# Kernel tuning notes

Hardware: AMD Instinct MI355X
Metric: run time of the kernel (lower is better)

Reference implementation:

```python
import jax, jax.numpy as jnp
import numpy as np

B, S, F, I, E, TOP_K, K, D, CLASSES = 2, 2048, 512, 1024, 8, 2, 7, 2, 8192
BETA = 0.9
INIT_SCALE = D ** -0.5


def setup_inputs() -> dict:
    key = jax.random.key(0)
    ks = jax.random.split(key, 10)
    s = lambda *shape: shape
    return {
        "inp": jax.random.randint(ks[0], (B, S), 0, CLASSES),
        "embed": jax.random.normal(ks[1], (CLASSES, 2 * F), jnp.float32) * 0.02,
        "gate_in_w": jax.random.normal(ks[2], (D, F, E), jnp.float32) * (F ** -0.5),
        "w_in": jax.random.normal(ks[3], (D, E, F, I), jnp.float32) * (F ** -0.5),
        "conv_w": jax.random.normal(ks[4], (D, I, I, K), jnp.float32) * ((I * K) ** -0.5),
        "gate_out_w": jax.random.normal(ks[5], (D, I, E), jnp.float32) * (I ** -0.5),
        "w_out": jax.random.normal(ks[6], (D, E, I, 3 * F), jnp.float32) * (I ** -0.5),
        "out_w": jax.random.normal(ks[7], (CLASSES, 2 * F), jnp.float32) * ((2 * F) ** -0.5),
        "out_b": jnp.zeros((CLASSES,), jnp.float32),
    }


def _moe(x, gate_w, expert_w):
    # x: [T, Fin]; NaiveGate top-k routing + grouped-GEMM combine.
    logits = x @ gate_w                                  # [T, E]
    top_vals, top_idx = jax.lax.top_k(logits, TOP_K)     # [T, k]
    scores = jax.nn.softmax(top_vals, axis=-1)           # softmax over selected experts
    n_exp = gate_w.shape[1]
    combine = jnp.sum(scores[:, :, None] * jax.nn.one_hot(top_idx, n_exp, dtype=x.dtype), axis=1)  # [T, E]
    y = jnp.einsum("tf,efo->teo", x, expert_w)           # dense all-expert eval
    return jnp.einsum("teo,te->to", y, combine)


def _norm(out):
    # custom norm over channel dim (dim 1 of [B, C, S])
    out = out - out.mean(axis=1, keepdims=True)
    c = out.shape[1]
    return out / (jnp.linalg.norm(out, axis=1, keepdims=True) * (c ** -0.5) + 1e-5)


def _cell(x, gate_in, win, cw, gate_out, wout, divisor):
    # x: [B, F, S]
    b, f, seq = x.shape
    t = x.transpose(0, 2, 1).reshape(b * seq, f)
    h = jax.nn.relu(_moe(t, gate_in, win))               # [T, I]
    h = h.reshape(b, seq, -1).transpose(0, 2, 1)         # [B, I, S]
    # causal depthwise-style conv (groups=1), left-pad K-1
    h = jax.lax.conv_general_dilated(h, cw, (1,), [(cw.shape[-1] - 1, 0)],
                                     dimension_numbers=("NCH", "OIH", "NCH"))
    h = jax.nn.relu(h)
    t2 = h.transpose(0, 2, 1).reshape(b * seq, -1)
    o = _moe(t2, gate_out, wout).reshape(b, seq, 3 * f).transpose(0, 2, 1)  # [B, 3F, S]
    depth_, scale, shift = jnp.split(o, 3, axis=1)
    cum = jnp.cumsum(depth_, axis=2)                      # running sum over sequence
    out = cum / divisor * scale + shift
    return _norm(out) * INIT_SCALE


def reference(inp, embed, gate_in_w, w_in, conv_w, gate_out_w, w_out, out_w, out_b):
    emb = embed[inp]                                      # [B, S, 2F]
    x = emb.transpose(0, 2, 1)                            # [B, 2F, S]
    x0, x1 = x[:, :F], x[:, F:]
    divisor = (jnp.arange(S, dtype=x.dtype) + 1.0)[None, None, :]
    for d in range(D):
        # momentum coupling with LinearAttentionCell
        f = _cell(x1, gate_in_w[d], w_in[d], conv_w[d], gate_out_w[d], w_out[d], divisor)
        y = x0 * BETA + f * (1.0 - BETA)
        x0, x1 = x1, y
        # additive coupling with Identity
        y = x0 + x1
        x0, x1 = x1, y
    out = jnp.concatenate([x0, x1], axis=1)               # [B, 2F, S]
    logits = jnp.einsum("bcs,kc->bks", out, out_w) + out_b[None, :, None]
    return logits
```

## Files before the change

### kernel.cpp

```cpp
#include <hip/hip_runtime.h>
#include <math.h>

typedef unsigned short u16;
typedef unsigned int   u32;

#define B_ 2
#define S_ 2048
#define F_ 512
#define I_ 1024
#define E_ 8
#define KW_ 7
#define D_ 2
#define CLASSES_ 8192
#define T_ (B_*S_)
#define SP_ (S_+6)
#define NSLOT_ 9216
#define GMAX_ 72

typedef __bf16 bf16x8 __attribute__((ext_vector_type(8)));
typedef float  f32x4  __attribute__((ext_vector_type(4)));

__device__ __forceinline__ u16 f2b(float f) {
    u32 x = __float_as_uint(f);
    return (u16)((x + 0x7fffu + ((x >> 16) & 1u)) >> 16);
}
__device__ __forceinline__ void fsplit(float v, u16& h, u16& l) {
    u16 hh = f2b(v);
    float hv = __uint_as_float(((u32)hh) << 16);
    h = hh;
    l = f2b(v - hv);
}

template<int N> __device__ __forceinline__ void waitvm() {
    asm volatile("s_waitcnt vmcnt(%0)" :: "n"(N) : "memory");
}

#define GLDS16(g, l) __builtin_amdgcn_global_load_lds( \
    (const __attribute__((address_space(1))) u32*)(g), \
    (__attribute__((address_space(3))) u32*)(l), 16, 0, 0)

__global__ void embed_k(const int* __restrict__ inp, const float* __restrict__ emb,
                        float* __restrict__ X0, float* __restrict__ X1)
{
    int t = blockIdx.x;
    int r = inp[t];
    const float* e = emb + (size_t)r * (2*F_);
    for (int c = threadIdx.x; c < F_; c += 256) {
        X0[(size_t)t*F_ + c] = e[c];
        X1[(size_t)t*F_ + c] = e[F_ + c];
    }
}

__global__ void initslot_k(int* __restrict__ stok, int* __restrict__ cnt)
{
    int i = blockIdx.x*256 + threadIdx.x;
    if (i < NSLOT_) stok[i] = -1;
    if (i < E_) cnt[i] = 0;
}

template<int MODE, int W>
__global__ __launch_bounds__(512) void gatev_k(const float* __restrict__ X,
                                               const float* __restrict__ X2,
                                               const float* __restrict__ GW,
                                               int2* __restrict__ e2, float2* __restrict__ w2,
                                               int* __restrict__ cnt)
{
    __shared__ float gw[W*E_];
    for (int i = threadIdx.x; i < W*E_; i += 512) {
        int f = i >> 3, e = i & 7;
        gw[e*W + f] = GW[i];
    }
    __syncthreads();
    int wv = threadIdx.x >> 6, l = threadIdx.x & 63;
    int t = blockIdx.x * 8 + wv;
    const float* xr  = X + (size_t)t * W;
    const float* x2r = MODE ? (X2 + (size_t)t * W) : nullptr;
    float a[8];
    #pragma unroll
    for (int e = 0; e < 8; e++) a[e] = 0.f;
    #pragma unroll
    for (int c = 0; c < W/256; c++) {
        int f = c*256 + l*4;
        float4 x = *(const float4*)(xr + f);
        if (MODE) {
            float4 y = *(const float4*)(x2r + f);
            x.x = fmaxf(x.x + y.x, 0.f); x.y = fmaxf(x.y + y.y, 0.f);
            x.z = fmaxf(x.z + y.z, 0.f); x.w = fmaxf(x.w + y.w, 0.f);
        }
        #pragma unroll
        for (int e = 0; e < 8; e++) {
            float4 g = *(const float4*)(gw + e*W + f);
            a[e] += x.x*g.x + x.y*g.y + x.z*g.z + x.w*g.w;
        }
    }
    #pragma unroll
    for (int e = 0; e < 8; e++) {
        #pragma unroll
        for (int off = 32; off; off >>= 1) a[e] += __shfl_xor(a[e], off);
    }
    if (l == 0) {
        float v0 = -3.4e38f, v1 = -3.4e38f; int i0 = 0, i1 = 0;
        #pragma unroll
        for (int k = 0; k < E_; k++) {
            float v = a[k];
            if (v > v0)      { v1 = v0; i1 = i0; v0 = v; i0 = k; }
            else if (v > v1) { v1 = v;  i1 = k; }
        }
        float ex = expf(v1 - v0);
        e2[t] = make_int2(i0, i1);
        w2[t] = make_float2(1.f/(1.f+ex), ex/(1.f+ex));
        atomicAdd(&cnt[i0], 1);
        atomicAdd(&cnt[i1], 1);
    }
}

__global__ __launch_bounds__(256) void schedscat_k(const int* __restrict__ cnt,
                                                   const int2* __restrict__ e2,
                                                   const float2* __restrict__ w2,
                                                   int4* __restrict__ s0, int4* __restrict__ s1,
                                                   int split,
                                                   int* __restrict__ stok, float* __restrict__ sw)
{
    __shared__ int lpos[E_];
    int tid = threadIdx.x;
    int nb[E_], slotst[E_], gst[E_];
    int poff = 0, g0 = 0, g1 = 0;
    #pragma unroll
    for (int e = 0; e < E_; e++) {
        int n = (cnt[e] + 127) >> 7;
        nb[e] = n;
        slotst[e] = poff;
        if (e < split) { gst[e] = g0; g0 += n; }
        else           { gst[e] = g1; g1 += n; }
        poff += n << 7;
    }
    if (tid < E_) lpos[tid] = slotst[tid];
    if (tid < GMAX_) {
        int4 en = make_int4(0,0,0,0);
        for (int e = 0; e < split; e++)
            if (tid >= gst[e] && tid < gst[e] + nb[e])
                en = make_int4(slotst[e] + (tid - gst[e])*128, e, 1, 0);
        s0[tid] = en;
    }
    if (split < E_ && tid >= 128 && tid < 128 + GMAX_) {
        int j = tid - 128;
        int4 en = make_int4(0,0,0,0);
        for (int e = split; e < E_; e++)
            if (j >= gst[e] && j < gst[e] + nb[e])
                en = make_int4(slotst[e] + (j - gst[e])*128, e - split, 1, 0);
        s1[j] = en;
    }
    __syncthreads();
    for (int t = tid; t < T_; t += 256) {
        int2 e = e2[t]; float2 w = w2[t];
        int p0 = atomicAdd(&lpos[e.x], 1);
        stok[p0] = t;          sw[p0] = w.x;
        int p1 = atomicAdd(&lpos[e.y], 1);
        stok[p1] = t | 4096;   sw[p1] = w.y;
    }
}

__global__ __launch_bounds__(256) void transp_k(const float* __restrict__ src0,
                                                u16* __restrict__ dh, u16* __restrict__ dl,
                                                int R, int C)
{
    __shared__ float tl[32][33];
    int z = blockIdx.z;
    const float* src = src0 + (size_t)z * R * C;
    size_t dbase = (size_t)z * R * C;
    int c0 = blockIdx.x * 32, r0 = blockIdx.y * 32;
    int tx = threadIdx.x & 31, ty = threadIdx.x >> 5;
    #pragma unroll
    for (int j = 0; j < 32; j += 8)
        tl[ty + j][tx] = src[(size_t)(r0 + ty + j) * C + c0 + tx];
    __syncthreads();
    #pragma unroll
    for (int j = 0; j < 32; j += 8) {
        u16 h, l; fsplit(tl[tx][ty + j], h, l);
        size_t idx = dbase + (size_t)(c0 + ty + j) * R + r0 + tx;
        dh[idx] = h; dl[idx] = l;
    }
}

__global__ __launch_bounds__(256) void convw_k(const float* __restrict__ src,
                                               u16* __restrict__ dh, u16* __restrict__ dl)
{
    __shared__ float row[KW_*I_];
    int o = blockIdx.x;
    const float* s = src + (size_t)o * (KW_*I_);
    for (int c = threadIdx.x; c < KW_*I_; c += 256) row[c] = s[c];
    __syncthreads();
    size_t base = (size_t)o * (KW_*I_);
    for (int j = threadIdx.x; j < KW_*I_; j += 256) {
        int kc = j >> 10, i = j & 1023;
        u16 h, l; fsplit(row[i*KW_ + kc], h, l);
        dh[base + j] = h; dl[base + j] = l;
    }
}

__global__ void split_k(const float* __restrict__ src, u16* __restrict__ dh, u16* __restrict__ dl)
{
    size_t i = ((size_t)blockIdx.x * 256 + threadIdx.x) * 4;
    float4 v = *(const float4*)(src + i);
    ushort4 oh, ol;
    fsplit(v.x, oh.x, ol.x); fsplit(v.y, oh.y, ol.y);
    fsplit(v.z, oh.z, ol.z); fsplit(v.w, oh.w, ol.w);
    *(ushort4*)(dh + i) = oh;
    *(ushort4*)(dl + i) = ol;
}

__global__ void hsplit_k(const float* __restrict__ Ha, const float* __restrict__ Hb,
                         u16* __restrict__ ph, u16* __restrict__ pl)
{
    int gid = blockIdx.x*256 + threadIdx.x;
    int eb = gid * 4;
    int t = eb >> 10, c = eb & 1023;
    float4 a = *(const float4*)(Ha + eb);
    float4 b = *(const float4*)(Hb + eb);
    ushort4 hh, ll;
    fsplit(fmaxf(a.x+b.x,0.f), hh.x, ll.x); fsplit(fmaxf(a.y+b.y,0.f), hh.y, ll.y);
    fsplit(fmaxf(a.z+b.z,0.f), hh.z, ll.z); fsplit(fmaxf(a.w+b.w,0.f), hh.w, ll.w);
    size_t row = (size_t)(t >> 11)*SP_ + 6 + (t & (S_-1));
    *(ushort4*)(ph + (row << 10) + c) = hh;
    *(ushort4*)(pl + (row << 10) + c) = ll;
}

__global__ void crelu_k(const float* __restrict__ a0, const float* __restrict__ a1,
                        u16* __restrict__ dh, u16* __restrict__ dl)
{
    size_t i = ((size_t)blockIdx.x * 256 + threadIdx.x) * 4;
    float4 a = *(const float4*)(a0 + i);
    float4 b = *(const float4*)(a1 + i);
    ushort4 hh, ll;
    fsplit(fmaxf(a.x+b.x,0.f), hh.x, ll.x); fsplit(fmaxf(a.y+b.y,0.f), hh.y, ll.y);
    fsplit(fmaxf(a.z+b.z,0.f), hh.z, ll.z); fsplit(fmaxf(a.w+b.w,0.f), hh.w, ll.w);
    *(ushort4*)(dh + i) = hh;
    *(ushort4*)(dl + i) = ll;
}

__global__ void hpadzero_k(u16* __restrict__ ph, u16* __restrict__ pl)
{
    int idx = blockIdx.x*256 + threadIdx.x;
    int b = idx / (6*I_);
    int rem = idx - b*(6*I_);
    size_t a = ((size_t)b*SP_ + (rem >> 10))*I_ + (rem & 1023);
    ph[a] = 0; pl[a] = 0;
}

enum { A_SPLIT=0, A_CONV=1, A_GATHER2=2 };
enum { EP_RANK=0, EP_DUAL=1, EP_FINAL=2 };

#define SBSZ(Pv) ((((Pv)==3)?16384:8192) + 8192*(((Pv)>=2)?2:1))

template<int AM, int EP, int PASSES>
__global__ __launch_bounds__(256, ((2*SBSZ(PASSES)) <= 32768) ? 4 : (((2*SBSZ(PASSES)) <= 49152) ? 3 : 2))
void mgemm(const void* __restrict__ A1, const void* __restrict__ A2,
           const u16* __restrict__ Bh, const u16* __restrict__ Bl,
           float* __restrict__ Ca, float* __restrict__ Cb,
           int N, int Kd, int ldb,
           const int4* __restrict__ sched, const int* __restrict__ stok,
           const float* __restrict__ sw, const float* __restrict__ bias)
{
    constexpr bool HAL = (PASSES==3);
    constexpr bool HBL = (PASSES>=2);
    constexpr int OAL  = 8192;
    constexpr int OBH  = (HAL ? 16384 : 8192);
    constexpr int OBL  = OBH + 8192;
    constexpr int SB   = OBH + 8192*(HBL ? 2 : 1);
    constexpr int NLOADS = 2*(HBL ? 2 : 1) + 2*(HAL ? 2 : 1);
    __shared__ uint4 ldsv[2*SB/16];
    char* lds = (char*)ldsv;

    const int tid  = threadIdx.x;
    const int lane = tid & 63, wid = tid >> 6;
    const int n0 = blockIdx.x * 128;

    int slot0 = 0, m0 = 0, koff = 0, kz = 0;
    const u16 *bhb = Bh, *blb = Bl;
    if (AM == A_GATHER2) {
        int4 sc = sched[blockIdx.y];
        if (!sc.z) return;
        slot0 = sc.x;
        size_t wo = (size_t)sc.y * N * ldb;
        bhb = Bh + wo; blb = Bl + wo;
    } else if (AM == A_CONV) {
        m0 = (blockIdx.y & 31) * 128;
        kz = blockIdx.y >> 5;
        koff = kz * Kd;
    } else {
        m0 = blockIdx.y * 128;
    }

    int srow[2], klog[2];
    #pragma unroll
    for (int c = 0; c < 2; c++) {
        int row = (tid >> 2) + c*64;
        srow[c] = row;
        klog[c] = ((tid & 3) ^ ((row >> 1) & 3)) << 3;
    }

    const u16 *bgh[2], *bgl[2];
    #pragma unroll
    for (int c = 0; c < 2; c++) {
        size_t off = (size_t)(n0 + srow[c]) * ldb + koff + klog[c];
        bgh[c] = bhb + off;
        bgl[c] = blb + off;
    }

    const u16 *a1p[2], *a2p[2];
    #pragma unroll
    for (int c = 0; c < 2; c++) {
        if (AM == A_SPLIT) {
            size_t off = (size_t)(m0 + srow[c]) * Kd + klog[c];
            a1p[c] = (const u16*)A1 + off;
            a2p[c] = (const u16*)A2 + off;
        } else if (AM == A_CONV) {
            int t = m0 + srow[c];
            size_t rb = (((size_t)(t >> 11)*SP_ + (t & (S_-1))) << 10) + koff + klog[c];
            a1p[c] = (const u16*)A1 + rb;
            a2p[c] = (const u16*)A2 + rb;
        } else {
            int s = stok[slot0 + srow[c]];
            int tk = (s < 0) ? 0 : (s & 4095);
            size_t off = (size_t)tk * Kd + klog[c];
            a1p[c] = (const u16*)A1 + off;
            a2p[c] = (const u16*)A2 + off;
        }
    }

    const int wr = wid >> 1, wc = wid & 1;
    const int l15 = lane & 15, kq = lane >> 4;
    int aoff[4], boff[4];
    #pragma unroll
    for (int m = 0; m < 4; m++) {
        int ra = wr*64 + m*16 + l15;
        aoff[m] = ra*64 + ((kq ^ ((ra >> 1) & 3)) << 4);
    }
    #pragma unroll
    for (int n = 0; n < 4; n++) {
        int rb = wc*64 + n*16 + l15;
        boff[n] = rb*64 + ((kq ^ ((rb >> 1) & 3)) << 4);
    }

    f32x4 acc[4][4];
    #pragma unroll
    for (int m = 0; m < 4; m++)
        #pragma unroll
        for (int n = 0; n < 4; n++) acc[m][n] = {0.f,0.f,0.f,0.f};

    const int nt = Kd >> 5;

#define STAGE_GL(K0, BB)                                                          \
    {                                                                             \
        _Pragma("unroll")                                                         \
        for (int c = 0; c < 2; c++) {                                             \
            GLDS16(bgh[c] + (K0), lds + (BB) + OBH + c*4096 + (wid<<10));         \
            if (HBL)                                                              \
                GLDS16(bgl[c] + (K0), lds + (BB) + OBL + c*4096 + (wid<<10));     \
        }                                                                         \
        _Pragma("unroll")                                                         \
        for (int c = 0; c < 2; c++) {                                             \
            GLDS16(a1p[c] + (K0), lds + (BB) + c*4096 + (wid<<10));               \
            if (HAL)                                                              \
                GLDS16(a2p[c] + (K0), lds + (BB) + OAL + c*4096 + (wid<<10));     \
        }                                                                         \
    }

    STAGE_GL(0, 0);
    STAGE_GL(32, SB);
    waitvm<NLOADS>();
    __builtin_amdgcn_s_barrier();

    for (int it = 0; it < nt; ++it) {
        const int bb = (it & 1) * SB;
        {
            bf16x8 ah[4], al[4], bhf[4], blf[4];
            #pragma unroll
            for (int m = 0; m < 4; m++) {
                ah[m] = *(const bf16x8*)(lds + bb + aoff[m]);
                if (HAL) al[m] = *(const bf16x8*)(lds + bb + OAL + aoff[m]);
            }
            #pragma unroll
            for (int n = 0; n < 4; n++) {
                bhf[n] = *(const bf16x8*)(lds + bb + OBH + boff[n]);
                if (HBL) blf[n] = *(const bf16x8*)(lds + bb + OBL + boff[n]);
            }
            #pragma unroll
            for (int m = 0; m < 4; m++)
                #pragma unroll
                for (int n = 0; n < 4; n++) {
                    acc[m][n] = __builtin_amdgcn_mfma_f32_16x16x32_bf16(ah[m], bhf[n], acc[m][n], 0, 0, 0);
                    if (HAL)
                        acc[m][n] = __builtin_amdgcn_mfma_f32_16x16x32_bf16(al[m], bhf[n], acc[m][n], 0, 0, 0);
                    if (HBL)
                        acc[m][n] = __builtin_amdgcn_mfma_f32_16x16x32_bf16(ah[m], blf[n], acc[m][n], 0, 0, 0);
                }
        }
        asm volatile("s_waitcnt lgkmcnt(0)" ::: "memory");
        __builtin_amdgcn_sched_barrier(0);
        __builtin_amdgcn_s_barrier();
        if (it + 2 < nt) {
            STAGE_GL((it + 2) << 5, bb);
            waitvm<NLOADS>();
            __builtin_amdgcn_s_barrier();
        } else if (it + 1 < nt) {
            waitvm<0>();
            __builtin_amdgcn_s_barrier();
        }
    }

    #pragma unroll
    for (int m = 0; m < 4; m++) {
        #pragma unroll
        for (int n = 0; n < 4; n++) {
            f32x4 v = acc[m][n];
            int rl0 = wr*64 + m*16 + (lane >> 4)*4;
            int col = n0 + wc*64 + n*16 + l15;
            #pragma unroll
            for (int j = 0; j < 4; j++) {
                float x = v[j];
                int rl = rl0 + j;
                if (EP == EP_RANK) {
                    int s = stok[slot0 + rl];
                    if (s >= 0) {
                        int tt = s & 4095;
                        float ww = sw[slot0 + rl];
                        float* dst = (s & 4096) ? Cb : Ca;
                        dst[(size_t)tt * N + col] = ww * x;
                    }
                } else if (EP == EP_DUAL) {
                    int r = m0 + rl;
                    float* dst = kz ? Cb : Ca;
                    dst[(size_t)r * N + col] = x;
                } else {
                    int r = m0 + rl;
                    x += bias[r];
                    int b = col >> 11, s = col & (S_-1);
                    Ca[(((size_t)(b*CLASSES_ + r)) << 11) + s] = x;
                }
            }
        }
    }
#undef STAGE_GL
}

#define SC_ 128
#define NCH_ (S_/SC_)
__global__ void cum1(const float* __restrict__ Oa, const float* __restrict__ Ob,
                     float* __restrict__ CS)
{
    int blk = blockIdx.x;
    int b = blk / NCH_, ch = blk % NCH_;
    int c = threadIdx.x;
    int s0 = ch * SC_;
    size_t base = ((size_t)(b*S_ + s0)) * (3*F_) + c;
    float sum = 0.f;
    for (int s = 0; s < SC_; s++) {
        size_t idx = base + (size_t)s * (3*F_);
        sum += Oa[idx] + Ob[idx];
    }
    CS[(size_t)blk * F_ + c] = sum;
}
__global__ void cum23(const float* __restrict__ Oa, const float* __restrict__ Ob,
                      const float* __restrict__ CS, float* __restrict__ FP)
{
    int blk = blockIdx.x;
    int b = blk / NCH_, ch = blk % NCH_;
    int c = threadIdx.x;
    float run = 0.f;
    for (int j = 0; j < ch; j++) run += CS[(size_t)(b*NCH_ + j) * F_ + c];
    int s0 = ch * SC_;
    for (int s = s0; s < s0 + SC_; s++) {
        size_t t = (size_t)b * S_ + s;
        size_t ro = t * (3*F_);
        run += Oa[ro + c] + Ob[ro + c];
        float scl = Oa[ro + F_ + c] + Ob[ro + F_ + c];
        float shf = Oa[ro + 2*F_ + c] + Ob[ro + 2*F_ + c];
        FP[t*F_ + c] = run / (float)(s + 1) * scl + shf;
    }
}

__global__ __launch_bounds__(256) void normupd_k(const float* __restrict__ FP,
                                                 float* __restrict__ X0, float* __restrict__ X1)
{
    __shared__ float sb[4];
    int t = blockIdx.x;
    const float* row = FP + (size_t)t * F_;
    int tid = threadIdx.x;
    float v0 = row[tid], v1 = row[tid + 256];
    float s = v0 + v1;
    #pragma unroll
    for (int off = 32; off; off >>= 1) s += __shfl_xor(s, off);
    int w = tid >> 6;
    if ((tid & 63) == 0) sb[w] = s;
    __syncthreads();
    float mean = (sb[0] + sb[1] + sb[2] + sb[3]) * (1.0f / F_);
    v0 -= mean; v1 -= mean;
    float q = v0*v0 + v1*v1;
    #pragma unroll
    for (int off = 32; off; off >>= 1) q += __shfl_xor(q, off);
    __syncthreads();
    if ((tid & 63) == 0) sb[w] = q;
    __syncthreads();
    float ss = sb[0] + sb[1] + sb[2] + sb[3];
    float denom = sqrtf(ss) * 0.04419417382415922f + 1e-5f;
    float sc = 0.70710678118654752f / denom;
    float f0 = v0 * sc, f1 = v1 * sc;
    size_t i0 = (size_t)t * F_ + tid, i1 = i0 + 256;
    float a0 = 0.9f * X0[i0] + 0.1f * f0;
    float a1 = 0.9f * X0[i1] + 0.1f * f1;
    X0[i0] = a0; X1[i0] += a0;
    X0[i1] = a1; X1[i1] += a1;
}

__global__ void concat_k(const float* __restrict__ X0, const float* __restrict__ X1,
                         u16* __restrict__ Xh, u16* __restrict__ Xl)
{
    int t = blockIdx.x;
    for (int c = threadIdx.x; c < F_; c += 256) {
        u16 h, l;
        fsplit(X0[(size_t)t*F_ + c], h, l);
        Xh[(size_t)t*(2*F_) + c] = h;      Xl[(size_t)t*(2*F_) + c] = l;
        fsplit(X1[(size_t)t*F_ + c], h, l);
        Xh[(size_t)t*(2*F_) + F_ + c] = h; Xl[(size_t)t*(2*F_) + F_ + c] = l;
    }
}

extern "C" void kernel_launch(void* const* d_in, const int* in_sizes, int n_in,
                              void* d_out, int out_size, void* d_ws, size_t ws_size,
                              hipStream_t stream)
{
    const int*   inp    = (const int*)  d_in[0];
    const float* embed  = (const float*)d_in[1];
    const float* gin_w  = (const float*)d_in[2];
    const float* w_in   = (const float*)d_in[3];
    const float* conv_w = (const float*)d_in[4];
    const float* gout_w = (const float*)d_in[5];
    const float* w_out  = (const float*)d_in[6];
    const float* out_w  = (const float*)d_in[7];
    const float* out_b  = (const float*)d_in[8];
    float* out = (float*)d_out;

    char* w = (char*)d_ws;
    auto alloc = [&](size_t bytes) { char* r = w; w += (bytes + 255) & ~(size_t)255; return r; };
    float* X0    = (float*)alloc((size_t)T_*F_*4);
    float* X1    = (float*)alloc((size_t)T_*F_*4);
    u16*   Hpadh = (u16*)  alloc((size_t)B_*SP_*I_*2);
    u16*   Hpadl = (u16*)  alloc((size_t)B_*SP_*I_*2);
    u16*   HCh   = (u16*)  alloc((size_t)T_*I_*2);
    u16*   HCl   = (u16*)  alloc((size_t)T_*I_*2);
    float* FP    = (float*)alloc((size_t)T_*F_*4);
    float* CS    = (float*)alloc((size_t)B_*NCH_*F_*4);
    char*  ar1   = alloc((size_t)T_*3*F_*4);
    char*  ar2   = alloc((size_t)T_*I_*4);
    char*  altr  = alloc((size_t)T_*3*F_*4);
    u16*   Wh    = (u16*)  alloc((size_t)I_*KW_*I_*2);
    u16*   Wl    = (u16*)  alloc((size_t)I_*KW_*I_*2);
    int2*  e2    = (int2*) alloc((size_t)T_*8);
    float2* w2   = (float2*)alloc((size_t)T_*8);
    int*   stok  = (int*)  alloc((size_t)NSLOT_*4);
    float* sw    = (float*)alloc((size_t)NSLOT_*4);
    int*   cnt   = (int*)  alloc(64);
    int4*  s0    = (int4*) alloc((size_t)GMAX_*16);
    int4*  s1    = (int4*) alloc((size_t)GMAX_*16);

    float* Ha  = (float*)ar1;
    float* Oa  = (float*)ar1;
    float* HC0 = (float*)ar2;
    float* Hb  = (float*)altr;
    float* HC1 = (float*)altr;
    float* Ob  = (float*)altr;
    u16*   X1h = (u16*)FP;
    u16*   X1l = X1h + (size_t)T_*F_;

    embed_k<<<T_, 256, 0, stream>>>(inp, embed, X0, X1);
    hpadzero_k<<<(B_*6*I_)/256, 256, 0, stream>>>(Hpadh, Hpadl);

    for (int d = 0; d < D_; ++d) {
        initslot_k<<<(NSLOT_+255)/256, 256, 0, stream>>>(stok, cnt);
        gatev_k<0, F_><<<T_/8, 512, 0, stream>>>(X1, nullptr, gin_w + (size_t)d*F_*E_, e2, w2, cnt);
        schedscat_k<<<1, 256, 0, stream>>>(cnt, e2, w2, s0, s1, 8, stok, sw);
        split_k<<<(T_*F_)/1024, 256, 0, stream>>>(X1, X1h, X1l);
        transp_k<<<dim3(I_/32, F_/32, E_), 256, 0, stream>>>(
            w_in + (size_t)d*E_*F_*I_, Wh, Wl, F_, I_);
        mgemm<A_GATHER2, EP_RANK, 3><<<dim3(I_/128, GMAX_), 256, 0, stream>>>(
            X1h, X1l, Wh, Wl, Ha, Hb, I_, F_, F_, s0, stok, sw, nullptr);
        hsplit_k<<<T_*I_/1024, 256, 0, stream>>>(Ha, Hb, Hpadh, Hpadl);

        convw_k<<<I_, 256, 0, stream>>>(conv_w + (size_t)d*I_*I_*KW_, Wh, Wl);
        mgemm<A_CONV, EP_DUAL, 3><<<dim3(I_/128, 64), 256, 0, stream>>>(
            Hpadh, Hpadl, Wh, Wl, HC0, HC1, I_, (KW_*I_)/2, KW_*I_, nullptr, nullptr, nullptr, nullptr);
        crelu_k<<<T_*I_/1024, 256, 0, stream>>>(HC0, HC1, HCh, HCl);

        initslot_k<<<(NSLOT_+255)/256, 256, 0, stream>>>(stok, cnt);
        gatev_k<1, I_><<<T_/8, 512, 0, stream>>>(HC0, HC1, gout_w + (size_t)d*I_*E_, e2, w2, cnt);
        schedscat_k<<<1, 256, 0, stream>>>(cnt, e2, w2, s0, s1, 4, stok, sw);
        for (int c = 0; c < 2; ++c) {
            transp_k<<<dim3((3*F_)/32, I_/32, 4), 256, 0, stream>>>(
                w_out + (size_t)d*E_*I_*(3*F_) + (size_t)c*4*I_*(3*F_), Wh, Wl, I_, 3*F_);
            const int4* sc = (c == 0) ? s0 : s1;
            if (d == 0)
                mgemm<A_GATHER2, EP_RANK, 3><<<dim3((3*F_)/128, GMAX_), 256, 0, stream>>>(
                    HCh, HCl, Wh, Wl, Oa, Ob, 3*F_, I_, I_, sc, stok, sw, nullptr);
            else
                mgemm<A_GATHER2, EP_RANK, 1><<<dim3((3*F_)/128, GMAX_), 256, 0, stream>>>(
                    HCh, HCl, Wh, Wl, Oa, Ob, 3*F_, I_, I_, sc, stok, sw, nullptr);
        }

        cum1<<<B_*NCH_, F_, 0, stream>>>(Oa, Ob, CS);
        cum23<<<B_*NCH_, F_, 0, stream>>>(Oa, Ob, CS, FP);
        normupd_k<<<T_, 256, 0, stream>>>(FP, X0, X1);
    }

    u16* Xch  = (u16*)ar1;
    u16* Xcl  = (u16*)(ar1 + (size_t)T_*(2*F_)*2);
    u16* OWh  = (u16*)ar2;
    u16* OWl  = Hpadh;

    concat_k<<<T_, 256, 0, stream>>>(X0, X1, Xch, Xcl);
    split_k<<<(CLASSES_*2*F_)/1024, 256, 0, stream>>>(out_w, OWh, OWl);
    mgemm<A_SPLIT, EP_FINAL, 2><<<dim3(T_/128, CLASSES_/128), 256, 0, stream>>>(
        OWh, OWl, Xch, Xcl, out, nullptr, T_, 2*F_, 2*F_, nullptr, nullptr, nullptr, out_b);
}
```

Baseline: 1.479 ms.

## Fuse gating with bf16 split, parallelize scatter, swizzle conv GEMM blocks, add MFMA priority

The gate kernels now also write the hi/lo bf16 split of their input, which removes the separate split_k and crelu_k passes. The single-block schedule+scatter kernel becomes a small schedule kernel plus a multi-block scatter kernel. The schedule kernel resets only the padding slots and the counters, so the per-layer initslot launches go away. The conv GEMM gets an XCD-aware block swizzle to improve L2 locality, and all GEMMs raise wave priority around the MFMA loop. The risks are atomic contention on the global position counters and whether the stale stok entries are handled correctly across calls.

```diff
diff --git a/kernel.cpp b/kernel.cpp
--- a/kernel.cpp
+++ b/kernel.cpp
@@ -58,38 +58,36 @@
     if (i < E_) cnt[i] = 0;
 }
 
-template<int MODE, int W>
-__global__ __launch_bounds__(512) void gatev_k(const float* __restrict__ X,
-                                               const float* __restrict__ X2,
-                                               const float* __restrict__ GW,
-                                               int2* __restrict__ e2, float2* __restrict__ w2,
-                                               int* __restrict__ cnt)
-{
-    __shared__ float gw[W*E_];
-    for (int i = threadIdx.x; i < W*E_; i += 512) {
+__global__ __launch_bounds__(512) void gatesplit1_k(const float* __restrict__ X,
+                                                    const float* __restrict__ GW,
+                                                    u16* __restrict__ Xh, u16* __restrict__ Xl,
+                                                    int2* __restrict__ e2, float2* __restrict__ w2,
+                                                    int* __restrict__ cnt)
+{
+    __shared__ float gw[F_*E_];
+    for (int i = threadIdx.x; i < F_*E_; i += 512) {
         int f = i >> 3, e = i & 7;
-        gw[e*W + f] = GW[i];
+        gw[e*F_ + f] = GW[i];
     }
     __syncthreads();
     int wv = threadIdx.x >> 6, l = threadIdx.x & 63;
     int t = blockIdx.x * 8 + wv;
-    const float* xr  = X + (size_t)t * W;
-    const float* x2r = MODE ? (X2 + (size_t)t * W) : nullptr;
+    const float* xr = X + (size_t)t * F_;
     float a[8];
     #pragma unroll
     for (int e = 0; e < 8; e++) a[e] = 0.f;
     #pragma unroll
-    for (int c = 0; c < W/256; c++) {
+    for (int c = 0; c < F_/256; c++) {
         int f = c*256 + l*4;
         float4 x = *(const float4*)(xr + f);
-        if (MODE) {
-            float4 y = *(const float4*)(x2r + f);
-            x.x = fmaxf(x.x + y.x, 0.f); x.y = fmaxf(x.y + y.y, 0.f);
-            x.z = fmaxf(x.z + y.z, 0.f); x.w = fmaxf(x.w + y.w, 0.f);
-        }
+        ushort4 oh, ol;
+        fsplit(x.x, oh.x, ol.x); fsplit(x.y, oh.y, ol.y);
+        fsplit(x.z, oh.z, ol.z); fsplit(x.w, oh.w, ol.w);
+        *(ushort4*)(Xh + (size_t)t*F_ + f) = oh;
+        *(ushort4*)(Xl + (size_t)t*F_ + f) = ol;
         #pragma unroll
         for (int e = 0; e < 8; e++) {
-            float4 g = *(const float4*)(gw + e*W + f);
+            float4 g = *(const float4*)(gw + e*F_ + f);
             a[e] += x.x*g.x + x.y*g.y + x.z*g.z + x.w*g.w;
         }
     }
@@ -114,50 +112,115 @@
     }
 }
 
-__global__ __launch_bounds__(256) void schedscat_k(const int* __restrict__ cnt,
-                                                   const int2* __restrict__ e2,
-                                                   const float2* __restrict__ w2,
-                                                   int4* __restrict__ s0, int4* __restrict__ s1,
-                                                   int split,
-                                                   int* __restrict__ stok, float* __restrict__ sw)
-{
-    __shared__ int lpos[E_];
+__global__ __launch_bounds__(512) void gatecrelu2_k(const float* __restrict__ A0,
+                                                    const float* __restrict__ A1v,
+                                                    const float* __restrict__ GW,
+                                                    u16* __restrict__ Hh, u16* __restrict__ Hl,
+                                                    int2* __restrict__ e2, float2* __restrict__ w2,
+                                                    int* __restrict__ cnt)
+{
+    __shared__ float gw[I_*E_];
+    for (int i = threadIdx.x; i < I_*E_; i += 512) {
+        int f = i >> 3, e = i & 7;
+        gw[e*I_ + f] = GW[i];
+    }
+    __syncthreads();
+    int wv = threadIdx.x >> 6, l = threadIdx.x & 63;
+    int t = blockIdx.x * 8 + wv;
+    const float* xr  = A0 + (size_t)t * I_;
+    const float* x2r = A1v + (size_t)t * I_;
+    float a[8];
+    #pragma unroll
+    for (int e = 0; e < 8; e++) a[e] = 0.f;
+    #pragma unroll
+    for (int c = 0; c < I_/256; c++) {
+        int f = c*256 + l*4;
+        float4 x = *(const float4*)(xr + f);
+        float4 y = *(const float4*)(x2r + f);
+        x.x = fmaxf(x.x + y.x, 0.f); x.y = fmaxf(x.y + y.y, 0.f);
+        x.z = fmaxf(x.z + y.z, 0.f); x.w = fmaxf(x.w + y.w, 0.f);
+        ushort4 oh, ol;
+        fsplit(x.x, oh.x, ol.x); fsplit(x.y, oh.y, ol.y);
+        fsplit(x.z, oh.z, ol.z); fsplit(x.w, oh.w, ol.w);
+        *(ushort4*)(Hh + (size_t)t*I_ + f) = oh;
+        *(ushort4*)(Hl + (size_t)t*I_ + f) = ol;
+        #pragma unroll
+        for (int e = 0; e < 8; e++) {
+            float4 g = *(const float4*)(gw + e*I_ + f);
+            a[e] += x.x*g.x + x.y*g.y + x.z*g.z + x.w*g.w;
+        }
+    }
+    #pragma unroll
+    for (int e = 0; e < 8; e++) {
+        #pragma unroll
+        for (int off = 32; off; off >>= 1) a[e] += __shfl_xor(a[e], off);
+    }
+    if (l == 0) {
+        float v0 = -3.4e38f, v1 = -3.4e38f; int i0 = 0, i1 = 0;
+        #pragma unroll
+        for (int k = 0; k < E_; k++) {
+            float v = a[k];
+            if (v > v0)      { v1 = v0; i1 = i0; v0 = v; i0 = k; }
+            else if (v > v1) { v1 = v;  i1 = k; }
+        }
+        float ex = expf(v1 - v0);
+        e2[t] = make_int2(i0, i1);
+        w2[t] = make_float2(1.f/(1.f+ex), ex/(1.f+ex));
+        atomicAdd(&cnt[i0], 1);
+        atomicAdd(&cnt[i1], 1);
+    }
+}
+
+__global__ __launch_bounds__(256) void sched_k(int* __restrict__ cnt, int* __restrict__ pos,
+                                               int4* __restrict__ s0, int4* __restrict__ s1,
+                                               int split, int* __restrict__ stok)
+{
     int tid = threadIdx.x;
-    int nb[E_], slotst[E_], gst[E_];
+    int nb[E_], slotst[E_], gst[E_], cn[E_];
     int poff = 0, g0 = 0, g1 = 0;
     #pragma unroll
     for (int e = 0; e < E_; e++) {
-        int n = (cnt[e] + 127) >> 7;
+        cn[e] = cnt[e];
+        int n = (cn[e] + 127) >> 7;
         nb[e] = n;
         slotst[e] = poff;
         if (e < split) { gst[e] = g0; g0 += n; }
         else           { gst[e] = g1; g1 += n; }
         poff += n << 7;
     }
-    if (tid < E_) lpos[tid] = slotst[tid];
-    if (tid < GMAX_) {
+    if (tid < E_) pos[tid] = slotst[tid];
+    for (int j = tid; j < GMAX_; j += 256) {
         int4 en = make_int4(0,0,0,0);
         for (int e = 0; e < split; e++)
-            if (tid >= gst[e] && tid < gst[e] + nb[e])
-                en = make_int4(slotst[e] + (tid - gst[e])*128, e, 1, 0);
-        s0[tid] = en;
-    }
-    if (split < E_ && tid >= 128 && tid < 128 + GMAX_) {
-        int j = tid - 128;
-        int4 en = make_int4(0,0,0,0);
-        for (int e = split; e < E_; e++)
             if (j >= gst[e] && j < gst[e] + nb[e])
-                en = make_int4(slotst[e] + (j - gst[e])*128, e - split, 1, 0);
-        s1[j] = en;
-    }
-    __syncthreads();
-    for (int t = tid; t < T_; t += 256) {
-        int2 e = e2[t]; float2 w = w2[t];
-        int p0 = atomicAdd(&lpos[e.x], 1);
-        stok[p0] = t;          sw[p0] = w.x;
-        int p1 = atomicAdd(&lpos[e.y], 1);
-        stok[p1] = t | 4096;   sw[p1] = w.y;
-    }
+                en = make_int4(slotst[e] + (j - gst[e])*128, e, 1, 0);
+        s0[j] = en;
+        if (split < E_) {
+            int4 en1 = make_int4(0,0,0,0);
+            for (int e = split; e < E_; e++)
+                if (j >= gst[e] && j < gst[e] + nb[e])
+                    en1 = make_int4(slotst[e] + (j - gst[e])*128, e - split, 1, 0);
+            s1[j] = en1;
+        }
+    }
+    #pragma unroll
+    for (int e = 0; e < E_; e++)
+        for (int i = slotst[e] + cn[e] + tid; i < slotst[e] + (nb[e] << 7); i += 256)
+            stok[i] = -1;
+    __syncthreads();
+    if (tid < E_) cnt[tid] = 0;
+}
+
+__global__ void scatter_k(const int2* __restrict__ e2, const float2* __restrict__ w2,
+                          int* __restrict__ pos, int* __restrict__ stok, float* __restrict__ sw)
+{
+    int t = blockIdx.x * 512 + threadIdx.x;
+    if (t >= T_) return;
+    int2 e = e2[t]; float2 w = w2[t];
+    int p0 = atomicAdd(&pos[e.x], 1);
+    stok[p0] = t;          sw[p0] = w.x;
+    int p1 = atomicAdd(&pos[e.y], 1);
+    stok[p1] = t | 4096;   sw[p1] = w.y;
 }
 
 __global__ __launch_bounds__(256) void transp_k(const float* __restrict__ src0,
@@ -225,19 +288,6 @@
     *(ushort4*)(pl + (row << 10) + c) = ll;
 }
 
-__global__ void crelu_k(const float* __restrict__ a0, const float* __restrict__ a1,
-                        u16* __restrict__ dh, u16* __restrict__ dl)
-{
-    size_t i = ((size_t)blockIdx.x * 256 + threadIdx.x) * 4;
-    float4 a = *(const float4*)(a0 + i);
-    float4 b = *(const float4*)(a1 + i);
-    ushort4 hh, ll;
-    fsplit(fmaxf(a.x+b.x,0.f), hh.x, ll.x); fsplit(fmaxf(a.y+b.y,0.f), hh.y, ll.y);
-    fsplit(fmaxf(a.z+b.z,0.f), hh.z, ll.z); fsplit(fmaxf(a.w+b.w,0.f), hh.w, ll.w);
-    *(ushort4*)(dh + i) = hh;
-    *(ushort4*)(dl + i) = ll;
-}
-
 __global__ void hpadzero_k(u16* __restrict__ ph, u16* __restrict__ pl)
 {
     int idx = blockIdx.x*256 + threadIdx.x;
@@ -252,7 +302,7 @@
 
 #define SBSZ(Pv) ((((Pv)==3)?16384:8192) + 8192*(((Pv)>=2)?2:1))
 
-template<int AM, int EP, int PASSES>
+template<int AM, int EP, int PASSES, int SWZ>
 __global__ __launch_bounds__(256, ((2*SBSZ(PASSES)) <= 32768) ? 4 : (((2*SBSZ(PASSES)) <= 49152) ? 3 : 2))
 void mgemm(const void* __restrict__ A1, const void* __restrict__ A2,
            const u16* __restrict__ Bh, const u16* __restrict__ Bl,
@@ -273,7 +323,7 @@
 
     const int tid  = threadIdx.x;
     const int lane = tid & 63, wid = tid >> 6;
-    const int n0 = blockIdx.x * 128;
+    int n0 = blockIdx.x * 128;
 
     int slot0 = 0, m0 = 0, koff = 0, kz = 0;
     const u16 *bhb = Bh, *blb = Bl;
@@ -284,9 +334,20 @@
         size_t wo = (size_t)sc.y * N * ldb;
         bhb = Bh + wo; blb = Bl + wo;
     } else if (AM == A_CONV) {
-        m0 = (blockIdx.y & 31) * 128;
-        kz = blockIdx.y >> 5;
-        koff = kz * Kd;
+        if (SWZ == 1) {
+            int fid = blockIdx.y * 8 + blockIdx.x;
+            int xcd = fid & 7, k = fid >> 3;
+            int mp = (xcd >> 1) * 8 + (k >> 3);
+            int np = (xcd & 1) * 8 + (k & 7);
+            m0 = mp * 128;
+            kz = np >> 3;
+            koff = kz * Kd;
+            n0 = (np & 7) * 128;
+        } else {
+            m0 = (blockIdx.y & 31) * 128;
+            kz = blockIdx.y >> 5;
+            koff = kz * Kd;
+        }
     } else {
         m0 = blockIdx.y * 128;
     }
@@ -385,6 +446,7 @@
                 bhf[n] = *(const bf16x8*)(lds + bb + OBH + boff[n]);
                 if (HBL) blf[n] = *(const bf16x8*)(lds + bb + OBL + boff[n]);
             }
+            __builtin_amdgcn_s_setprio(1);
             #pragma unroll
             for (int m = 0; m < 4; m++)
                 #pragma unroll
@@ -395,6 +457,7 @@
                     if (HBL)
                         acc[m][n] = __builtin_amdgcn_mfma_f32_16x16x32_bf16(ah[m], blf[n], acc[m][n], 0, 0, 0);
                 }
+            __builtin_amdgcn_s_setprio(0);
         }
         asm volatile("s_waitcnt lgkmcnt(0)" ::: "memory");
         __builtin_amdgcn_sched_barrier(0);
@@ -561,6 +624,7 @@
     int*   stok  = (int*)  alloc((size_t)NSLOT_*4);
     float* sw    = (float*)alloc((size_t)NSLOT_*4);
     int*   cnt   = (int*)  alloc(64);
+    int*   pos   = (int*)  alloc(64);
     int4*  s0    = (int4*) alloc((size_t)GMAX_*16);
     int4*  s1    = (int4*) alloc((size_t)GMAX_*16);
 
@@ -575,35 +639,36 @@
 
     embed_k<<<T_, 256, 0, stream>>>(inp, embed, X0, X1);
     hpadzero_k<<<(B_*6*I_)/256, 256, 0, stream>>>(Hpadh, Hpadl);
+    initslot_k<<<(NSLOT_+255)/256, 256, 0, stream>>>(stok, cnt);
 
     for (int d = 0; d < D_; ++d) {
-        initslot_k<<<(NSLOT_+255)/256, 256, 0, stream>>>(stok, cnt);
-        gatev_k<0, F_><<<T_/8, 512, 0, stream>>>(X1, nullptr, gin_w + (size_t)d*F_*E_, e2, w2, cnt);
-        schedscat_k<<<1, 256, 0, stream>>>(cnt, e2, w2, s0, s1, 8, stok, sw);
-        split_k<<<(T_*F_)/1024, 256, 0, stream>>>(X1, X1h, X1l);
+        gatesplit1_k<<<T_/8, 512, 0, stream>>>(X1, gin_w + (size_t)d*F_*E_,
+                                               X1h, X1l, e2, w2, cnt);
+        sched_k<<<1, 256, 0, stream>>>(cnt, pos, s0, s1, 8, stok);
+        scatter_k<<<T_/512, 512, 0, stream>>>(e2, w2, pos, stok, sw);
         transp_k<<<dim3(I_/32, F_/32, E_), 256, 0, stream>>>(
             w_in + (size_t)d*E_*F_*I_, Wh, Wl, F_, I_);
-        mgemm<A_GATHER2, EP_RANK, 3><<<dim3(I_/128, GMAX_), 256, 0, stream>>>(
+        mgemm<A_GATHER2, EP_RANK, 3, 0><<<dim3(I_/128, GMAX_), 256, 0, stream>>>(
             X1h, X1l, Wh, Wl, Ha, Hb, I_, F_, F_, s0, stok, sw, nullptr);
         hsplit_k<<<T_*I_/1024, 256, 0, stream>>>(Ha, Hb, Hpadh, Hpadl);
 
         convw_k<<<I_, 256, 0, stream>>>(conv_w + (size_t)d*I_*I_*KW_, Wh, Wl);
-        mgemm<A_CONV, EP_DUAL, 3><<<dim3(I_/128, 64), 256, 0, stream>>>(
+        mgemm<A_CONV, EP_DUAL, 3, 1><<<dim3(8, 64), 256, 0, stream>>>(
             Hpadh, Hpadl, Wh, Wl, HC0, HC1, I_, (KW_*I_)/2, KW_*I_, nullptr, nullptr, nullptr, nullptr);
-        crelu_k<<<T_*I_/1024, 256, 0, stream>>>(HC0, HC1, HCh, HCl);
-
-        initslot_k<<<(NSLOT_+255)/256, 256, 0, stream>>>(stok, cnt);
-        gatev_k<1, I_><<<T_/8, 512, 0, stream>>>(HC0, HC1, gout_w + (size_t)d*I_*E_, e2, w2, cnt);
-        schedscat_k<<<1, 256, 0, stream>>>(cnt, e2, w2, s0, s1, 4, stok, sw);
+
+        gatecrelu2_k<<<T_/8, 512, 0, stream>>>(HC0, HC1, gout_w + (size_t)d*I_*E_,
+                                               HCh, HCl, e2, w2, cnt);
+        sched_k<<<1, 256, 0, stream>>>(cnt, pos, s0, s1, 4, stok);
+        scatter_k<<<T_/512, 512, 0, stream>>>(e2, w2, pos, stok, sw);
         for (int c = 0; c < 2; ++c) {
             transp_k<<<dim3((3*F_)/32, I_/32, 4), 256, 0, stream>>>(
                 w_out + (size_t)d*E_*I_*(3*F_) + (size_t)c*4*I_*(3*F_), Wh, Wl, I_, 3*F_);
             const int4* sc = (c == 0) ? s0 : s1;
             if (d == 0)
-                mgemm<A_GATHER2, EP_RANK, 3><<<dim3((3*F_)/128, GMAX_), 256, 0, stream>>>(
+                mgemm<A_GATHER2, EP_RANK, 3, 0><<<dim3((3*F_)/128, GMAX_), 256, 0, stream>>>(
                     HCh, HCl, Wh, Wl, Oa, Ob, 3*F_, I_, I_, sc, stok, sw, nullptr);
             else
-                mgemm<A_GATHER2, EP_RANK, 1><<<dim3((3*F_)/128, GMAX_), 256, 0, stream>>>(
+                mgemm<A_GATHER2, EP_RANK, 1, 0><<<dim3((3*F_)/128, GMAX_), 256, 0, stream>>>(
                     HCh, HCl, Wh, Wl, Oa, Ob, 3*F_, I_, I_, sc, stok, sw, nullptr);
         }
 
@@ -619,6 +684,6 @@
 
     concat_k<<<T_, 256, 0, stream>>>(X0, X1, Xch, Xcl);
     split_k<<<(CLASSES_*2*F_)/1024, 256, 0, stream>>>(out_w, OWh, OWl);
-    mgemm<A_SPLIT, EP_FINAL, 2><<<dim3(T_/128, CLASSES_/128), 256, 0, stream>>>(
+    mgemm<A_SPLIT, EP_FINAL, 2, 0><<<dim3(T_/128, CLASSES_/128), 256, 0, stream>>>(
         OWh, OWl, Xch, Xcl, out, nullptr, T_, 2*F_, 2*F_, nullptr, nullptr, nullptr, out_b);
 }
```

After: 1.589 ms. +7.4%, slower.
